# Optimization experiments

Hardware: AMD Instinct MI355X
Metric: run time of the kernel (lower is better)

The kernel has to match this reference:

```python
import jax, jax.numpy as jnp
import numpy as np

B, N, F = 32, 1024, 7
HID, HID_GLO, MLP_H, OUT = 256, 8, 64, 8
THRESHOLD = 0.3


def setup_inputs() -> dict:
    key = jax.random.key(0)
    ks = jax.random.split(key, 16)
    def lin(k, fan_out, fan_in):
        # xavier-uniform-like init
        lim = (6.0 / (fan_in + fan_out)) ** 0.5
        return jax.random.uniform(k, (fan_out, fan_in), jnp.float32, -lim, lim)
    return {
        "x": jax.random.normal(ks[0], (B, N, F), jnp.float32),
        "W1": lin(ks[1], HID, 2),   "b1": jnp.zeros((HID,), jnp.float32),
        "W2": lin(ks[2], HID, HID), "b2": jnp.zeros((HID,), jnp.float32),
        "Wfc": lin(ks[3], HID, HID), "bfc": jnp.zeros((HID,), jnp.float32),
        "Wg": lin(ks[4], HID_GLO, 2), "bg": jnp.zeros((HID_GLO,), jnp.float32),
        "Wm0": lin(ks[5], MLP_H, N * F), "bm0": jnp.zeros((MLP_H,), jnp.float32),
        "Wm1": lin(ks[6], MLP_H, MLP_H), "bm1": jnp.zeros((MLP_H,), jnp.float32),
        "Wp": lin(ks[7], OUT, MLP_H + HID + HID_GLO), "bp": jnp.zeros((OUT,), jnp.float32),
    }


def reference(x, W1, b1, W2, b2, Wfc, bfc, Wg, bg, Wm0, bm0, Wm1, bm1, Wp, bp):
    # --- GCN branch (torch code detaches node features & adjacency) ---
    pts = jax.lax.stop_gradient(x[:, :, 1:3])                     # [B,N,2]
    diff = pts[:, :, None, :] - pts[:, None, :, :]                # [B,N,N,2]
    dist = jnp.sqrt(jnp.sum(diff * diff, axis=-1))                # [B,N,N]
    adj = (dist < THRESHOLD).astype(x.dtype)                      # [B,N,N]
    dinv = 1.0 / jnp.sqrt(jnp.sum(adj, axis=-1))                  # [B,N] (>=1, self-loop)
    nadj = dinv[:, :, None] * adj * dinv[:, None, :]              # D^-1/2 A D^-1/2
    h = jax.nn.relu(jnp.einsum('bij,bjd->bid', nadj, pts) @ W1.T + b1)   # [B,N,256]
    g = jnp.einsum('bij,bjh->bih', nadj, h) @ W2.T + b2                  # [B,N,256]
    gcn_en = jnp.mean(g, axis=1) @ Wfc.T + bfc                    # [B,256]

    # --- global branch (torch code uses .item() -> constants) ---
    v = jax.lax.stop_gradient(x[:, :, 1:5])                       # [B,N,4]
    avg_speed = jnp.mean(jnp.linalg.norm(v[:, :, 2:4], axis=-1), axis=1)  # [B]
    density = 1.0 / jnp.max(dist, axis=(1, 2))                    # [B] (v3 == pts)
    glo_in = jnp.stack([avg_speed, density], axis=-1)             # [B,2]
    glo_en = jax.nn.relu(glo_in @ Wg.T + bg)                      # [B,8]

    # --- MLP branch on flattened x ---
    xf = x.reshape(x.shape[0], -1)                                # [B, N*F]
    xf = jax.nn.relu(xf @ Wm0.T + bm0)
    xf = jax.nn.relu(xf @ Wm1.T + bm1)                            # [B,64]

    out = jnp.concatenate([xf, gcn_en, glo_en], axis=1) @ Wp.T + bp  # [B,8]
    return out
```

## Files before the change

### kernel.cpp

```cpp
#include <hip/hip_runtime.h>

#define BB 32
#define NN 1024
#define FF 7
#define HID 256
#define MLPH 64
#define OUTN 8
#define CATN (MLPH + HID + 8)

__device__ __forceinline__ float wave_sum(float v) {
#pragma unroll
    for (int m = 32; m >= 1; m >>= 1) v += __shfl_xor(v, m, 64);
    return v;
}
__device__ __forceinline__ float wave_max(float v) {
#pragma unroll
    for (int m = 32; m >= 1; m >>= 1) v = fmaxf(v, __shfl_xor(v, m, 64));
    return v;
}

__global__ __launch_bounds__(1024, 8) void kA(const float* __restrict__ x,
                                              const float* __restrict__ Wm0,
                                              const float* __restrict__ W2,
                                              const float* __restrict__ b2,
                                              const float* __restrict__ Wfc,
                                              const float* __restrict__ bfc,
                                              const float* __restrict__ Wp,
                                              float* __restrict__ deg,
                                              float* __restrict__ bmaxp,
                                              float* __restrict__ spd,
                                              float* __restrict__ mlp_p,
                                              float* __restrict__ E,
                                              float* __restrict__ cE) {
    __shared__ __align__(16) float l0[NN];
    __shared__ __align__(16) float l1[NN];
    __shared__ __align__(16) float red[NN];
    __shared__ float wred[16];
    int blk = blockIdx.x, tid = threadIdx.x, lane = tid & 63, w = tid >> 6;
    if (blk < 512) {
        int b = blk >> 4, jg = blk & 15;
        const float* xb = x + b * (NN * FF);
        l0[tid] = xb[tid * FF + 1];
        l1[tid] = xb[tid * FF + 2];
        __syncthreads();
        int j = jg * 64 + lane;
        float pj0 = l0[j], pj1 = l1[j];
        const float4* v0p = (const float4*)&l0[w * 64];
        const float4* v1p = (const float4*)&l1[w * 64];
        unsigned degv = 0u;
        float mx = 0.f;
#pragma unroll 4
        for (int g = 0; g < 16; ++g) {
            float4 v0 = v0p[g], v1 = v1p[g];
            float dxa = pj0 - v0.x, dya = pj1 - v1.x;
            float dxb = pj0 - v0.y, dyb = pj1 - v1.y;
            float dxc = pj0 - v0.z, dyc = pj1 - v1.z;
            float dxd = pj0 - v0.w, dyd = pj1 - v1.w;
            float da = fmaf(dya, dya, dxa * dxa);
            float db = fmaf(dyb, dyb, dxb * dxb);
            float dc = fmaf(dyc, dyc, dxc * dxc);
            float dd = fmaf(dyd, dyd, dxd * dxd);
            degv += (da <= 0.09f);
            degv += (db <= 0.09f);
            degv += (dc <= 0.09f);
            degv += (dd <= 0.09f);
            mx = fmaxf(fmaxf(mx, fmaxf(da, db)), fmaxf(dc, dd));
        }
        red[tid] = (float)degv;
        mx = wave_max(mx);
        if (lane == 0) wred[w] = mx;
        __syncthreads();
        if (tid < 64) {
            float s = 0.f;
#pragma unroll
            for (int kk = 0; kk < 16; ++kk) s += red[kk * 64 + tid];
            deg[b * NN + jg * 64 + tid] = s;
        }
        if (tid == 0) {
            float m = wred[0];
#pragma unroll
            for (int i = 1; i < 16; ++i) m = fmaxf(m, wred[i]);
            bmaxp[b * 16 + jg] = m;
        }
        if (w == 1) {
            int n = jg * 64 + lane;
            float vx = xb[n * FF + 3], vy = xb[n * FF + 4];
            float sp = sqrtf(fmaf(vx, vx, vy * vy));
            sp = wave_sum(sp);
            if (lane == 0) spd[b * 16 + jg] = sp;
        }
        {
            int id = blk * 16 + w;
            int mb = id >> 8, mh = (id >> 2) & 63, mc = id & 3;
            const float4* wr = (const float4*)(Wm0 + mh * (NN * FF) + mc * 1792);
            const float4* xr = (const float4*)(x + mb * (NN * FF) + mc * 1792);
            float4 a4 = {0.f, 0.f, 0.f, 0.f};
#pragma unroll
            for (int it = 0; it < 7; ++it) {
                float4 wv = wr[it * 64 + lane];
                float4 xv = xr[it * 64 + lane];
                a4.x = fmaf(wv.x, xv.x, a4.x);
                a4.y = fmaf(wv.y, xv.y, a4.y);
                a4.z = fmaf(wv.z, xv.z, a4.z);
                a4.w = fmaf(wv.w, xv.w, a4.w);
            }
            float s = (a4.x + a4.y) + (a4.z + a4.w);
            s = wave_sum(s);
            if (lane == 0) mlp_p[id] = s;
        }
    } else {
        int o = blk - 512;
        if (tid < HID) l0[tid] = Wp[o * CATN + MLPH + tid];
        __syncthreads();
        if (tid < HID) {
            float a = 0.f;
#pragma unroll 8
            for (int m = 0; m < HID; ++m) a = fmaf(l0[m], Wfc[m * HID + tid], a);
            l1[tid] = a;
            red[tid] = l0[tid] * bfc[tid];
        }
        __syncthreads();
        if (tid < HID) {
            float e = 0.f;
#pragma unroll 8
            for (int k = 0; k < HID; ++k) e = fmaf(l1[k], W2[k * HID + tid], e);
            E[o * HID + tid] = e;
            float c = fmaf(l1[tid], b2[tid], red[tid]);
            c = wave_sum(c);
            if (lane == 0) wred[w] = c;
        }
        __syncthreads();
        if (tid == 0) cE[o] = wred[0] + wred[1] + wred[2] + wred[3];
    }
}

__global__ __launch_bounds__(1024, 8) void kB(const float* __restrict__ x,
                                              const float* __restrict__ deg,
                                              float* __restrict__ q0,
                                              float* __restrict__ q1,
                                              float* __restrict__ wj) {
    __shared__ __align__(16) float l0[NN];
    __shared__ __align__(16) float l1[NN];
    __shared__ __align__(16) float di[NN];
    __shared__ __align__(16) float r0[NN];
    __shared__ __align__(16) float r1[NN];
    __shared__ __align__(16) float r2[NN];
    int blk = blockIdx.x, tid = threadIdx.x, lane = tid & 63, w = tid >> 6;
    int b = blk >> 4, jg = blk & 15;
    const float* xb = x + b * (NN * FF);
    l0[tid] = xb[tid * FF + 1];
    l1[tid] = xb[tid * FF + 2];
    di[tid] = 1.0f / sqrtf(deg[b * NN + tid]);
    __syncthreads();
    int j = jg * 64 + lane;
    float pj0 = l0[j], pj1 = l1[j];
    const float4* v0p = (const float4*)&l0[w * 64];
    const float4* v1p = (const float4*)&l1[w * 64];
    const float4* vdp = (const float4*)&di[w * 64];
    float a0 = 0.f, a1 = 0.f, as = 0.f;
#pragma unroll 4
    for (int g = 0; g < 16; ++g) {
        float4 v0 = v0p[g], v1 = v1p[g], vd = vdp[g];
        float dxa = pj0 - v0.x, dya = pj1 - v1.x;
        float dxb = pj0 - v0.y, dyb = pj1 - v1.y;
        float dxc = pj0 - v0.z, dyc = pj1 - v1.z;
        float dxd = pj0 - v0.w, dyd = pj1 - v1.w;
        float da = fmaf(dya, dya, dxa * dxa);
        float db = fmaf(dyb, dyb, dxb * dxb);
        float dc = fmaf(dyc, dyc, dxc * dxc);
        float dd = fmaf(dyd, dyd, dxd * dxd);
        float ta = (da <= 0.09f) ? vd.x : 0.0f;
        float tb = (db <= 0.09f) ? vd.y : 0.0f;
        float tc = (dc <= 0.09f) ? vd.z : 0.0f;
        float td = (dd <= 0.09f) ? vd.w : 0.0f;
        a0 = fmaf(ta, v0.x, a0); a1 = fmaf(ta, v1.x, a1); as += ta;
        a0 = fmaf(tb, v0.y, a0); a1 = fmaf(tb, v1.y, a1); as += tb;
        a0 = fmaf(tc, v0.z, a0); a1 = fmaf(tc, v1.z, a1); as += tc;
        a0 = fmaf(td, v0.w, a0); a1 = fmaf(td, v1.w, a1); as += td;
    }
    r0[tid] = a0; r1[tid] = a1; r2[tid] = as;
    __syncthreads();
    if (tid < 64) {
        float s0 = 0.f, s1 = 0.f, ss = 0.f;
#pragma unroll
        for (int kk = 0; kk < 16; ++kk) {
            s0 += r0[kk * 64 + tid];
            s1 += r1[kk * 64 + tid];
            ss += r2[kk * 64 + tid];
        }
        int jj = jg * 64 + tid;
        float dj = di[jj];
        q0[b * NN + jj] = dj * s0;
        q1[b * NN + jj] = dj * s1;
        wj[b * NN + jj] = dj * ss * (1.0f / NN);
    }
}

__global__ __launch_bounds__(1024, 4) void kF(const float* __restrict__ q0,
                                              const float* __restrict__ q1,
                                              const float* __restrict__ wj,
                                              const float* __restrict__ W1,
                                              const float* __restrict__ b1,
                                              const float* __restrict__ Wg,
                                              const float* __restrict__ bg,
                                              const float* __restrict__ Wm1,
                                              const float* __restrict__ bm1,
                                              const float* __restrict__ Wp,
                                              const float* __restrict__ bp,
                                              const float* __restrict__ bm0,
                                              const float* __restrict__ mlp_p,
                                              const float* __restrict__ bmaxp,
                                              const float* __restrict__ spd,
                                              const float* __restrict__ E,
                                              const float* __restrict__ cE,
                                              float* __restrict__ out) {
    __shared__ __align__(16) float sq0[NN];
    __shared__ __align__(16) float sq1[NN];
    __shared__ __align__(16) float sw[NN];
    __shared__ __align__(16) float hpp[4][HID];
    __shared__ __align__(16) float hs[HID];
    __shared__ float sx1[MLPH];
    __shared__ float sxf2[MLPH];
    __shared__ float sglo[8];
    int b = blockIdx.x, tid = threadIdx.x;
    sq0[tid] = q0[b * NN + tid];
    sq1[tid] = q1[b * NN + tid];
    sw[tid]  = wj[b * NN + tid];
    if (tid >= 448 && tid < 512) {
        int h = tid - 448;
        float4 p = *(const float4*)&mlp_p[b * 256 + h * 4];
        sx1[h] = fmaxf(((p.x + p.y) + (p.z + p.w)) + bm0[h], 0.f);
    }
    __syncthreads();
    {
        int h = tid & 255, jq = tid >> 8;
        float w10 = W1[h * 2], w11 = W1[h * 2 + 1], bb = b1[h];
        float acc = 0.f;
        const float4* q0v4 = (const float4*)&sq0[jq * 256];
        const float4* q1v4 = (const float4*)&sq1[jq * 256];
        const float4* wv4  = (const float4*)&sw[jq * 256];
#pragma unroll 4
        for (int g = 0; g < 64; ++g) {
            float4 q0v = q0v4[g], q1v = q1v4[g], wv = wv4[g];
            acc = fmaf(wv.x, fmaxf(fmaf(q1v.x, w11, fmaf(q0v.x, w10, bb)), 0.f), acc);
            acc = fmaf(wv.y, fmaxf(fmaf(q1v.y, w11, fmaf(q0v.y, w10, bb)), 0.f), acc);
            acc = fmaf(wv.z, fmaxf(fmaf(q1v.z, w11, fmaf(q0v.z, w10, bb)), 0.f), acc);
            acc = fmaf(wv.w, fmaxf(fmaf(q1v.w, w11, fmaf(q0v.w, w10, bb)), 0.f), acc);
        }
        hpp[jq][h] = acc;
    }
    __syncthreads();
    if (tid < HID) {
        hs[tid] = hpp[0][tid] + hpp[1][tid] + hpp[2][tid] + hpp[3][tid];
    } else if (tid < HID + MLPH) {
        int t = tid - HID;
        float a = bm1[t];
        const float* wv = Wm1 + t * MLPH;
#pragma unroll
        for (int k = 0; k < MLPH; ++k) a = fmaf(wv[k], sx1[k], a);
        sxf2[t] = fmaxf(a, 0.f);
    } else if (tid < HID + MLPH + 8) {
        int t = tid - HID - MLPH;
        float mx = 0.f, sp = 0.f;
#pragma unroll
        for (int g = 0; g < 16; ++g) {
            mx = fmaxf(mx, bmaxp[b * 16 + g]);
            sp += spd[b * 16 + g];
        }
        float avg  = sp * (1.0f / NN);
        float dens = 1.0f / sqrtf(mx);
        sglo[t] = fmaxf(fmaf(Wg[t * 2], avg, fmaf(Wg[t * 2 + 1], dens, bg[t])), 0.f);
    }
    __syncthreads();
    if (tid < 512) {
        int o = tid >> 6, lane = tid & 63;
        const float* Eo = E + o * HID;
        float a = Eo[lane] * hs[lane];
        a = fmaf(Eo[lane + 64],  hs[lane + 64],  a);
        a = fmaf(Eo[lane + 128], hs[lane + 128], a);
        a = fmaf(Eo[lane + 192], hs[lane + 192], a);
        a = fmaf(Wp[o * CATN + lane], sxf2[lane], a);
        a = wave_sum(a);
        if (lane == 0) {
            const float* wg = Wp + o * CATN + MLPH + HID;
#pragma unroll
            for (int g = 0; g < 8; ++g) a = fmaf(wg[g], sglo[g], a);
            out[b * OUTN + o] = a + cE[o] + bp[o];
        }
    }
}

extern "C" void kernel_launch(void* const* d_in, const int* in_sizes, int n_in,
                              void* d_out, int out_size, void* d_ws, size_t ws_size,
                              hipStream_t stream) {
    const float* x   = (const float*)d_in[0];
    const float* W1  = (const float*)d_in[1];
    const float* b1  = (const float*)d_in[2];
    const float* W2  = (const float*)d_in[3];
    const float* b2  = (const float*)d_in[4];
    const float* Wfc = (const float*)d_in[5];
    const float* bfc = (const float*)d_in[6];
    const float* Wg  = (const float*)d_in[7];
    const float* bg  = (const float*)d_in[8];
    const float* Wm0 = (const float*)d_in[9];
    const float* bm0 = (const float*)d_in[10];
    const float* Wm1 = (const float*)d_in[11];
    const float* bm1 = (const float*)d_in[12];
    const float* Wp  = (const float*)d_in[13];
    const float* bp  = (const float*)d_in[14];
    float* out = (float*)d_out;
    float* ws  = (float*)d_ws;

    float* deg   = ws;
    float* q0    = ws + 32768;
    float* q1    = ws + 65536;
    float* wj    = ws + 98304;
    float* mlp_p = ws + 131072;
    float* bmaxp = ws + 139264;
    float* spd   = ws + 139776;
    float* E     = ws + 140288;
    float* cE    = ws + 142336;

    kA<<<520, 1024, 0, stream>>>(x, Wm0, W2, b2, Wfc, bfc, Wp,
                                 deg, bmaxp, spd, mlp_p, E, cE);
    kB<<<512, 1024, 0, stream>>>(x, deg, q0, q1, wj);
    kF<<<BB,  1024, 0, stream>>>(q0, q1, wj, W1, b1, Wg, bg, Wm1, bm1, Wp, bp,
                                 bm0, mlp_p, bmaxp, spd, E, cE, out);
}
```

Baseline: 132.4 us.

## Process two target nodes per thread in pairwise kernels and split MLP blocks

```diff
diff --git a/kernel.cpp b/kernel.cpp
--- a/kernel.cpp
+++ b/kernel.cpp
@@ -19,7 +19,7 @@
     return v;
 }
 
-__global__ __launch_bounds__(1024, 8) void kA(const float* __restrict__ x,
+__global__ __launch_bounds__(1024, 4) void kA(const float* __restrict__ x,
                                               const float* __restrict__ Wm0,
                                               const float* __restrict__ W2,
                                               const float* __restrict__ b2,
@@ -34,82 +34,101 @@
                                               float* __restrict__ cE) {
     __shared__ __align__(16) float l0[NN];
     __shared__ __align__(16) float l1[NN];
-    __shared__ __align__(16) float red[NN];
+    __shared__ __align__(16) float s2[NN];
+    __shared__ __align__(16) float s3[NN];
     __shared__ float wred[16];
     int blk = blockIdx.x, tid = threadIdx.x, lane = tid & 63, w = tid >> 6;
-    if (blk < 512) {
-        int b = blk >> 4, jg = blk & 15;
+    if (blk < 256) {
+        int b = blk >> 3, jg = blk & 7;
         const float* xb = x + b * (NN * FF);
         l0[tid] = xb[tid * FF + 1];
         l1[tid] = xb[tid * FF + 2];
         __syncthreads();
-        int j = jg * 64 + lane;
-        float pj0 = l0[j], pj1 = l1[j];
+        int jA = jg * 128 + lane, jB = jA + 64;
+        float pj0a = l0[jA], pj1a = l1[jA];
+        float pj0b = l0[jB], pj1b = l1[jB];
         const float4* v0p = (const float4*)&l0[w * 64];
         const float4* v1p = (const float4*)&l1[w * 64];
-        unsigned degv = 0u;
+        unsigned dA = 0u, dB = 0u;
         float mx = 0.f;
 #pragma unroll 4
         for (int g = 0; g < 16; ++g) {
             float4 v0 = v0p[g], v1 = v1p[g];
-            float dxa = pj0 - v0.x, dya = pj1 - v1.x;
-            float dxb = pj0 - v0.y, dyb = pj1 - v1.y;
-            float dxc = pj0 - v0.z, dyc = pj1 - v1.z;
-            float dxd = pj0 - v0.w, dyd = pj1 - v1.w;
-            float da = fmaf(dya, dya, dxa * dxa);
-            float db = fmaf(dyb, dyb, dxb * dxb);
-            float dc = fmaf(dyc, dyc, dxc * dxc);
-            float dd = fmaf(dyd, dyd, dxd * dxd);
-            degv += (da <= 0.09f);
-            degv += (db <= 0.09f);
-            degv += (dc <= 0.09f);
-            degv += (dd <= 0.09f);
-            mx = fmaxf(fmaxf(mx, fmaxf(da, db)), fmaxf(dc, dd));
-        }
-        red[tid] = (float)degv;
+            float dx, dy, d2a, d2b;
+            dx = pj0a - v0.x; dy = pj1a - v1.x; d2a = fmaf(dy, dy, dx * dx);
+            dx = pj0b - v0.x; dy = pj1b - v1.x; d2b = fmaf(dy, dy, dx * dx);
+            dA += (d2a <= 0.09f); dB += (d2b <= 0.09f);
+            mx = fmaxf(mx, fmaxf(d2a, d2b));
+            dx = pj0a - v0.y; dy = pj1a - v1.y; d2a = fmaf(dy, dy, dx * dx);
+            dx = pj0b - v0.y; dy = pj1b - v1.y; d2b = fmaf(dy, dy, dx * dx);
+            dA += (d2a <= 0.09f); dB += (d2b <= 0.09f);
+            mx = fmaxf(mx, fmaxf(d2a, d2b));
+            dx = pj0a - v0.z; dy = pj1a - v1.z; d2a = fmaf(dy, dy, dx * dx);
+            dx = pj0b - v0.z; dy = pj1b - v1.z; d2b = fmaf(dy, dy, dx * dx);
+            dA += (d2a <= 0.09f); dB += (d2b <= 0.09f);
+            mx = fmaxf(mx, fmaxf(d2a, d2b));
+            dx = pj0a - v0.w; dy = pj1a - v1.w; d2a = fmaf(dy, dy, dx * dx);
+            dx = pj0b - v0.w; dy = pj1b - v1.w; d2b = fmaf(dy, dy, dx * dx);
+            dA += (d2a <= 0.09f); dB += (d2b <= 0.09f);
+            mx = fmaxf(mx, fmaxf(d2a, d2b));
+        }
+        s2[tid] = (float)dA;
+        s3[tid] = (float)dB;
         mx = wave_max(mx);
         if (lane == 0) wred[w] = mx;
         __syncthreads();
         if (tid < 64) {
             float s = 0.f;
 #pragma unroll
-            for (int kk = 0; kk < 16; ++kk) s += red[kk * 64 + tid];
-            deg[b * NN + jg * 64 + tid] = s;
+            for (int kk = 0; kk < 16; ++kk) s += s2[kk * 64 + tid];
+            deg[b * NN + jg * 128 + tid] = s;
+        } else if (tid < 128) {
+            int t = tid - 64;
+            float s = 0.f;
+#pragma unroll
+            for (int kk = 0; kk < 16; ++kk) s += s3[kk * 64 + t];
+            deg[b * NN + jg * 128 + 64 + t] = s;
         }
         if (tid == 0) {
             float m = wred[0];
 #pragma unroll
             for (int i = 1; i < 16; ++i) m = fmaxf(m, wred[i]);
-            bmaxp[b * 16 + jg] = m;
-        }
-        if (w == 1) {
-            int n = jg * 64 + lane;
-            float vx = xb[n * FF + 3], vy = xb[n * FF + 4];
+            bmaxp[b * 8 + jg] = m;
+        }
+        if (jg == 0) {
+            float vx = xb[tid * FF + 3], vy = xb[tid * FF + 4];
             float sp = sqrtf(fmaf(vx, vx, vy * vy));
             sp = wave_sum(sp);
-            if (lane == 0) spd[b * 16 + jg] = sp;
-        }
-        {
-            int id = blk * 16 + w;
-            int mb = id >> 8, mh = (id >> 2) & 63, mc = id & 3;
-            const float4* wr = (const float4*)(Wm0 + mh * (NN * FF) + mc * 1792);
-            const float4* xr = (const float4*)(x + mb * (NN * FF) + mc * 1792);
-            float4 a4 = {0.f, 0.f, 0.f, 0.f};
-#pragma unroll
-            for (int it = 0; it < 7; ++it) {
-                float4 wv = wr[it * 64 + lane];
-                float4 xv = xr[it * 64 + lane];
-                a4.x = fmaf(wv.x, xv.x, a4.x);
-                a4.y = fmaf(wv.y, xv.y, a4.y);
-                a4.z = fmaf(wv.z, xv.z, a4.z);
-                a4.w = fmaf(wv.w, xv.w, a4.w);
+            __syncthreads();
+            if (lane == 0) wred[w] = sp;
+            __syncthreads();
+            if (tid == 0) {
+                float s = 0.f;
+#pragma unroll
+                for (int i = 0; i < 16; ++i) s += wred[i];
+                spd[b] = s;
             }
-            float s = (a4.x + a4.y) + (a4.z + a4.w);
-            s = wave_sum(s);
-            if (lane == 0) mlp_p[id] = s;
-        }
+        }
+    } else if (blk < 384) {
+        int gid = (blk - 256) * 16 + w;
+        int b = gid >> 6, h = gid & 63;
+        const float4* wr = (const float4*)(Wm0 + h * (NN * FF));
+        const float4* xr = (const float4*)(x + b * (NN * FF));
+        float4 a4 = {0.f, 0.f, 0.f, 0.f};
+#pragma unroll 7
+        for (int it = 0; it < 28; ++it) {
+            float4 wv = wr[it * 64 + lane];
+            float4 xv = xr[it * 64 + lane];
+            a4.x = fmaf(wv.x, xv.x, a4.x);
+            a4.y = fmaf(wv.y, xv.y, a4.y);
+            a4.z = fmaf(wv.z, xv.z, a4.z);
+            a4.w = fmaf(wv.w, xv.w, a4.w);
+        }
+        float s = (a4.x + a4.y) + (a4.z + a4.w);
+        s = wave_sum(s);
+        if (lane == 0) mlp_p[gid] = s;
     } else {
-        int o = blk - 512;
+        int o = blk - 384;
         if (tid < HID) l0[tid] = Wp[o * CATN + MLPH + tid];
         __syncthreads();
         if (tid < HID) {
@@ -117,7 +136,7 @@
 #pragma unroll 8
             for (int m = 0; m < HID; ++m) a = fmaf(l0[m], Wfc[m * HID + tid], a);
             l1[tid] = a;
-            red[tid] = l0[tid] * bfc[tid];
+            s2[tid] = l0[tid] * bfc[tid];
         }
         __syncthreads();
         if (tid < HID) {
@@ -125,7 +144,7 @@
 #pragma unroll 8
             for (int k = 0; k < HID; ++k) e = fmaf(l1[k], W2[k * HID + tid], e);
             E[o * HID + tid] = e;
-            float c = fmaf(l1[tid], b2[tid], red[tid]);
+            float c = fmaf(l1[tid], b2[tid], s2[tid]);
             c = wave_sum(c);
             if (lane == 0) wred[w] = c;
         }
@@ -134,7 +153,7 @@
     }
 }
 
-__global__ __launch_bounds__(1024, 8) void kB(const float* __restrict__ x,
+__global__ __launch_bounds__(1024, 4) void kB(const float* __restrict__ x,
                                               const float* __restrict__ deg,
                                               float* __restrict__ q0,
                                               float* __restrict__ q1,
@@ -142,57 +161,76 @@
     __shared__ __align__(16) float l0[NN];
     __shared__ __align__(16) float l1[NN];
     __shared__ __align__(16) float di[NN];
-    __shared__ __align__(16) float r0[NN];
-    __shared__ __align__(16) float r1[NN];
-    __shared__ __align__(16) float r2[NN];
+    __shared__ __align__(16) float r0a[NN];
+    __shared__ __align__(16) float r1a[NN];
+    __shared__ __align__(16) float r2a[NN];
+    __shared__ __align__(16) float r0b[NN];
+    __shared__ __align__(16) float r1b[NN];
+    __shared__ __align__(16) float r2b[NN];
     int blk = blockIdx.x, tid = threadIdx.x, lane = tid & 63, w = tid >> 6;
-    int b = blk >> 4, jg = blk & 15;
+    int b = blk >> 3, jg = blk & 7;
     const float* xb = x + b * (NN * FF);
     l0[tid] = xb[tid * FF + 1];
     l1[tid] = xb[tid * FF + 2];
     di[tid] = 1.0f / sqrtf(deg[b * NN + tid]);
     __syncthreads();
-    int j = jg * 64 + lane;
-    float pj0 = l0[j], pj1 = l1[j];
+    int jA = jg * 128 + lane, jB = jA + 64;
+    float pj0a = l0[jA], pj1a = l1[jA];
+    float pj0b = l0[jB], pj1b = l1[jB];
     const float4* v0p = (const float4*)&l0[w * 64];
     const float4* v1p = (const float4*)&l1[w * 64];
     const float4* vdp = (const float4*)&di[w * 64];
-    float a0 = 0.f, a1 = 0.f, as = 0.f;
+    float a0a = 0.f, a1a = 0.f, asa = 0.f;
+    float a0b = 0.f, a1b = 0.f, asb = 0.f;
 #pragma unroll 4
     for (int g = 0; g < 16; ++g) {
         float4 v0 = v0p[g], v1 = v1p[g], vd = vdp[g];
-        float dxa = pj0 - v0.x, dya = pj1 - v1.x;
-        float dxb = pj0 - v0.y, dyb = pj1 - v1.y;
-        float dxc = pj0 - v0.z, dyc = pj1 - v1.z;
-        float dxd = pj0 - v0.w, dyd = pj1 - v1.w;
-        float da = fmaf(dya, dya, dxa * dxa);
-        float db = fmaf(dyb, dyb, dxb * dxb);
-        float dc = fmaf(dyc, dyc, dxc * dxc);
-        float dd = fmaf(dyd, dyd, dxd * dxd);
-        float ta = (da <= 0.09f) ? vd.x : 0.0f;
-        float tb = (db <= 0.09f) ? vd.y : 0.0f;
-        float tc = (dc <= 0.09f) ? vd.z : 0.0f;
-        float td = (dd <= 0.09f) ? vd.w : 0.0f;
-        a0 = fmaf(ta, v0.x, a0); a1 = fmaf(ta, v1.x, a1); as += ta;
-        a0 = fmaf(tb, v0.y, a0); a1 = fmaf(tb, v1.y, a1); as += tb;
-        a0 = fmaf(tc, v0.z, a0); a1 = fmaf(tc, v1.z, a1); as += tc;
-        a0 = fmaf(td, v0.w, a0); a1 = fmaf(td, v1.w, a1); as += td;
-    }
-    r0[tid] = a0; r1[tid] = a1; r2[tid] = as;
-    __syncthreads();
-    if (tid < 64) {
+        float dx, dy, d2, t;
+        dx = pj0a - v0.x; dy = pj1a - v1.x; d2 = fmaf(dy, dy, dx * dx);
+        t = (d2 <= 0.09f) ? vd.x : 0.0f;
+        a0a = fmaf(t, v0.x, a0a); a1a = fmaf(t, v1.x, a1a); asa += t;
+        dx = pj0b - v0.x; dy = pj1b - v1.x; d2 = fmaf(dy, dy, dx * dx);
+        t = (d2 <= 0.09f) ? vd.x : 0.0f;
+        a0b = fmaf(t, v0.x, a0b); a1b = fmaf(t, v1.x, a1b); asb += t;
+        dx = pj0a - v0.y; dy = pj1a - v1.y; d2 = fmaf(dy, dy, dx * dx);
+        t = (d2 <= 0.09f) ? vd.y : 0.0f;
+        a0a = fmaf(t, v0.y, a0a); a1a = fmaf(t, v1.y, a1a); asa += t;
+        dx = pj0b - v0.y; dy = pj1b - v1.y; d2 = fmaf(dy, dy, dx * dx);
+        t = (d2 <= 0.09f) ? vd.y : 0.0f;
+        a0b = fmaf(t, v0.y, a0b); a1b = fmaf(t, v1.y, a1b); asb += t;
+        dx = pj0a - v0.z; dy = pj1a - v1.z; d2 = fmaf(dy, dy, dx * dx);
+        t = (d2 <= 0.09f) ? vd.z : 0.0f;
+        a0a = fmaf(t, v0.z, a0a); a1a = fmaf(t, v1.z, a1a); asa += t;
+        dx = pj0b - v0.z; dy = pj1b - v1.z; d2 = fmaf(dy, dy, dx * dx);
+        t = (d2 <= 0.09f) ? vd.z : 0.0f;
+        a0b = fmaf(t, v0.z, a0b); a1b = fmaf(t, v1.z, a1b); asb += t;
+        dx = pj0a - v0.w; dy = pj1a - v1.w; d2 = fmaf(dy, dy, dx * dx);
+        t = (d2 <= 0.09f) ? vd.w : 0.0f;
+        a0a = fmaf(t, v0.w, a0a); a1a = fmaf(t, v1.w, a1a); asa += t;
+        dx = pj0b - v0.w; dy = pj1b - v1.w; d2 = fmaf(dy, dy, dx * dx);
+        t = (d2 <= 0.09f) ? vd.w : 0.0f;
+        a0b = fmaf(t, v0.w, a0b); a1b = fmaf(t, v1.w, a1b); asb += t;
+    }
+    r0a[tid] = a0a; r1a[tid] = a1a; r2a[tid] = asa;
+    r0b[tid] = a0b; r1b[tid] = a1b; r2b[tid] = asb;
+    __syncthreads();
+    if (tid < 128) {
+        int t = tid & 63;
+        const float* R0 = (tid < 64) ? r0a : r0b;
+        const float* R1 = (tid < 64) ? r1a : r1b;
+        const float* R2 = (tid < 64) ? r2a : r2b;
+        int j = jg * 128 + ((tid < 64) ? 0 : 64) + t;
         float s0 = 0.f, s1 = 0.f, ss = 0.f;
 #pragma unroll
         for (int kk = 0; kk < 16; ++kk) {
-            s0 += r0[kk * 64 + tid];
-            s1 += r1[kk * 64 + tid];
-            ss += r2[kk * 64 + tid];
-        }
-        int jj = jg * 64 + tid;
-        float dj = di[jj];
-        q0[b * NN + jj] = dj * s0;
-        q1[b * NN + jj] = dj * s1;
-        wj[b * NN + jj] = dj * ss * (1.0f / NN);
+            s0 += R0[kk * 64 + t];
+            s1 += R1[kk * 64 + t];
+            ss += R2[kk * 64 + t];
+        }
+        float dj = di[j];
+        q0[b * NN + j] = dj * s0;
+        q1[b * NN + j] = dj * s1;
+        wj[b * NN + j] = dj * ss * (1.0f / NN);
     }
 }
 
@@ -228,8 +266,7 @@
     sw[tid]  = wj[b * NN + tid];
     if (tid >= 448 && tid < 512) {
         int h = tid - 448;
-        float4 p = *(const float4*)&mlp_p[b * 256 + h * 4];
-        sx1[h] = fmaxf(((p.x + p.y) + (p.z + p.w)) + bm0[h], 0.f);
+        sx1[h] = fmaxf(mlp_p[b * MLPH + h] + bm0[h], 0.f);
     }
     __syncthreads();
     {
@@ -261,13 +298,10 @@
         sxf2[t] = fmaxf(a, 0.f);
     } else if (tid < HID + MLPH + 8) {
         int t = tid - HID - MLPH;
-        float mx = 0.f, sp = 0.f;
-#pragma unroll
-        for (int g = 0; g < 16; ++g) {
-            mx = fmaxf(mx, bmaxp[b * 16 + g]);
-            sp += spd[b * 16 + g];
-        }
-        float avg  = sp * (1.0f / NN);
+        float mx = 0.f;
+#pragma unroll
+        for (int g = 0; g < 8; ++g) mx = fmaxf(mx, bmaxp[b * 8 + g]);
+        float avg  = spd[b] * (1.0f / NN);
         float dens = 1.0f / sqrtf(mx);
         sglo[t] = fmaxf(fmaf(Wg[t * 2], avg, fmaf(Wg[t * 2 + 1], dens, bg[t])), 0.f);
     }
@@ -316,14 +350,14 @@
     float* q1    = ws + 65536;
     float* wj    = ws + 98304;
     float* mlp_p = ws + 131072;
-    float* bmaxp = ws + 139264;
-    float* spd   = ws + 139776;
-    float* E     = ws + 140288;
-    float* cE    = ws + 142336;
-
-    kA<<<520, 1024, 0, stream>>>(x, Wm0, W2, b2, Wfc, bfc, Wp,
+    float* bmaxp = ws + 133120;
+    float* spd   = ws + 133376;
+    float* E     = ws + 133408;
+    float* cE    = ws + 135456;
+
+    kA<<<392, 1024, 0, stream>>>(x, Wm0, W2, b2, Wfc, bfc, Wp,
                                  deg, bmaxp, spd, mlp_p, E, cE);
-    kB<<<512, 1024, 0, stream>>>(x, deg, q0, q1, wj);
+    kB<<<256, 1024, 0, stream>>>(x, deg, q0, q1, wj);
     kF<<<BB,  1024, 0, stream>>>(q0, q1, wj, W1, b1, Wg, bg, Wm1, bm1, Wp, bp,
                                  bm0, mlp_p, bmaxp, spd, E, cE, out);
 }
```

Result: faster. 129.6 us (-2.1%).
